# Kernel tuning notes

Measured on AMD Instinct MI355X. Metric: run time of the kernel, lower is better.

Reference implementation:

```python
import jax, jax.numpy as jnp
import numpy as np

N, E, D_IN, HID, OUT, H = 50000, 800000, 64, 128, 128, 8


def _lin(key, fan_in, fan_out, bias=True):
    k1, k2 = jax.random.split(key)
    W = jax.random.normal(k1, (fan_in, fan_out), jnp.float32) / np.sqrt(fan_in)
    if bias:
        b = jax.random.normal(k2, (fan_out,), jnp.float32) * 0.01
        return W, b
    return (W,)


def setup_inputs() -> dict:
    key = jax.random.key(0)
    ks = jax.random.split(key, 40)
    inp = {
        "x": jax.random.normal(ks[0], (N, D_IN), jnp.float32),
        "edge_index": jax.random.randint(ks[1], (2, E), 0, N, jnp.int64),
        "edge_attr": jax.random.normal(ks[2], (E, D_IN), jnp.float32),
    }
    dims = [(D_IN, HID), (HID, HID), (HID, OUT)]  # (in, heads*out_ch) per layer
    ki = 3
    for l, (di, do) in enumerate(dims):
        inp[f"Wq{l}"], inp[f"bq{l}"] = _lin(ks[ki], di, do); ki += 1
        inp[f"Wk{l}"], inp[f"bk{l}"] = _lin(ks[ki], di, do); ki += 1
        inp[f"Wv{l}"], inp[f"bv{l}"] = _lin(ks[ki], di, do); ki += 1
        (inp[f"We{l}"],) = _lin(ks[ki], D_IN, do, bias=False); ki += 1
        inp[f"Ws{l}"], inp[f"bs{l}"] = _lin(ks[ki], di, do); ki += 1
    for l in range(2):
        inp[f"g{l}"] = jnp.ones((HID,), jnp.float32)
        inp[f"be{l}"] = jnp.zeros((HID,), jnp.float32)
    return inp


def _transformer_conv(x, src, dst, edge_attr, Wq, bq, Wk, bk, Wv, bv, We, Ws, bs):
    n = x.shape[0]
    hc = Wq.shape[1]
    c = hc // H
    q = (x @ Wq + bq).reshape(n, H, c)
    k = (x @ Wk + bk).reshape(n, H, c)
    v = (x @ Wv + bv).reshape(n, H, c)
    e = (edge_attr @ We).reshape(-1, H, c)  # [E,H,c]
    ke = k[src] + e                          # edge-wise key + edge proj
    alpha = jnp.einsum("ehc,ehc->eh", q[dst], ke) / jnp.sqrt(jnp.float32(c))
    m = jax.ops.segment_max(alpha, dst, num_segments=n)
    m = jnp.where(jnp.isfinite(m), m, 0.0)
    p = jnp.exp(alpha - m[dst])
    s = jax.ops.segment_sum(p, dst, num_segments=n)
    a = p / (s[dst] + 1e-16)                 # segment softmax over in-edges
    msg = (v[src] + e) * a[..., None]
    out = jax.ops.segment_sum(msg, dst, num_segments=n).reshape(n, hc)
    return out + x @ Ws + bs                 # root/skip connection


def _bn(x, g, b):
    mu = jnp.mean(x, axis=0)
    var = jnp.mean(jnp.square(x - mu), axis=0)
    return g * (x - mu) * jax.lax.rsqrt(var + 1e-5) + b


def reference(x, edge_index, edge_attr,
              Wq0, bq0, Wk0, bk0, Wv0, bv0, We0, Ws0, bs0,
              Wq1, bq1, Wk1, bk1, Wv1, bv1, We1, Ws1, bs1,
              Wq2, bq2, Wk2, bk2, Wv2, bv2, We2, Ws2, bs2,
              g0, be0, g1, be1):
    src, dst = edge_index[0], edge_index[1]
    h = _transformer_conv(x, src, dst, edge_attr, Wq0, bq0, Wk0, bk0, Wv0, bv0, We0, Ws0, bs0)
    h = jax.nn.relu(_bn(h, g0, be0))
    h = _transformer_conv(h, src, dst, edge_attr, Wq1, bq1, Wk1, bk1, Wv1, bv1, We1, Ws1, bs1)
    h = jax.nn.relu(_bn(h, g1, be1))
    h = _transformer_conv(h, src, dst, edge_attr, Wq2, bq2, Wk2, bk2, Wv2, bv2, We2, Ws2, bs2)
    return h, edge_attr
```

## Files before the change

### kernel.cpp

```cpp
#include <hip/hip_runtime.h>
#include <hip/hip_bf16.h>

typedef __attribute__((ext_vector_type(8))) short short8;
typedef __attribute__((ext_vector_type(4))) float f32x4;
typedef unsigned short ushort_t;
typedef __attribute__((ext_vector_type(2))) unsigned short ushort2v;

static __device__ __forceinline__ ushort_t f2bf(float x) {
    __hip_bfloat16 h = __float2bfloat16(x);
    return *(ushort_t*)&h;
}
static __device__ __forceinline__ float bflo(unsigned int u) { return __uint_as_float(u << 16); }
static __device__ __forceinline__ float bfhi(unsigned int u) { return __uint_as_float(u & 0xffff0000u); }
static __device__ __forceinline__ float bfu(ushort_t u) { return __uint_as_float((unsigned int)u << 16); }


__global__ void hist_kernel(const int* __restrict__ dst, int E, int* __restrict__ hist) {
    int i = blockIdx.x * blockDim.x + threadIdx.x;
    if (i < E) atomicAdd(&hist[dst[i]], 1);
}

__global__ __launch_bounds__(1024) void scan_block_kernel(
    const int* __restrict__ hist, int n, int* __restrict__ row_ptr, int* __restrict__ bsums)
{
    __shared__ int lds[1024];
    int tid = threadIdx.x;
    int i = blockIdx.x * 1024 + tid;
    int vv = (i < n) ? hist[i] : 0;
    lds[tid] = vv;
    __syncthreads();
    for (int off = 1; off < 1024; off <<= 1) {
        int t = (tid >= off) ? lds[tid - off] : 0;
        __syncthreads();
        lds[tid] += t;
        __syncthreads();
    }
    if (i < n) row_ptr[i] = lds[tid] - vv;
    if (tid == 1023) bsums[blockIdx.x] = lds[1023];
}

__global__ void scan_tops_kernel(int* __restrict__ bsums, int nb) {
    if (threadIdx.x == 0 && blockIdx.x == 0) {
        int run = 0;
        for (int i = 0; i < nb; i++) { int t = bsums[i]; bsums[i] = run; run += t; }
    }
}

__global__ __launch_bounds__(256) void scan_add_kernel(
    const int* __restrict__ bsums, int n, int total,
    int* __restrict__ row_ptr, int* __restrict__ cursor)
{
    int i = blockIdx.x * blockDim.x + threadIdx.x;
    if (i < n) {
        int vv = row_ptr[i] + bsums[i >> 10];
        row_ptr[i] = vv;
        cursor[i] = vv;
    }
    if (i == 0) row_ptr[n] = total;
}

__global__ void scatter_kernel(const int* __restrict__ src, const int* __restrict__ dst, int E,
                               int* __restrict__ cursor, int* __restrict__ eid, int* __restrict__ srcs) {
    int i = blockIdx.x * blockDim.x + threadIdx.x;
    if (i < E) {
        int d = dst[i];
        int pos = atomicAdd(&cursor[d], 1);
        eid[pos] = i;
        srcs[pos] = src[i];
    }
}

__global__ __launch_bounds__(256) void permute_ea_kernel(
    const float* __restrict__ edge_attr, const int* __restrict__ eid, int E,
    ushort_t* __restrict__ ea)
{
    int idx = blockIdx.x * blockDim.x + threadIdx.x;
    if (idx >= E * 8) return;
    int j = idx >> 3, seg = idx & 7;
    int rsrc = eid[j];
    const float* s = edge_attr + (size_t)rsrc * 64 + seg * 8;
    float4 f0 = *(const float4*)s;
    float4 f1 = *(const float4*)(s + 4);
    short8 o;
    o[0] = f2bf(f0.x); o[1] = f2bf(f0.y); o[2] = f2bf(f0.z); o[3] = f2bf(f0.w);
    o[4] = f2bf(f1.x); o[5] = f2bf(f1.y); o[6] = f2bf(f1.z); o[7] = f2bf(f1.w);
    *(short8*)(ea + (size_t)j * 64 + seg * 8) = o;
}

__global__ __launch_bounds__(256) void pack_Wnode_kernel(
    const float* __restrict__ Wq, const float* __restrict__ Wk,
    const float* __restrict__ Wv, const float* __restrict__ Ws,
    int DI, ushort_t* __restrict__ dst)
{
    int NKF = DI >> 5;
    int total = DI * 512;
    int idx = blockIdx.x * blockDim.x + threadIdx.x;
    if (idx >= total) return;
    int j = idx & 7;
    int lane = (idx >> 3) & 63;
    int rest = idx >> 9;
    int kf = rest % NKF;
    int t = rest / NKF;
    int kdim = kf * 32 + (lane >> 4) * 8 + j;
    int ncol = t * 16 + (lane & 15);
    const float* W = (ncol < 128) ? Wq : (ncol < 256) ? Wk : (ncol < 384) ? Wv : Ws;
    dst[idx] = f2bf(W[kdim * 128 + (ncol & 127)]);
}

__global__ __launch_bounds__(256) void pack_bias_kernel(
    const float* __restrict__ bq, const float* __restrict__ bk,
    const float* __restrict__ bv, const float* __restrict__ bs,
    float* __restrict__ dst)
{
    int i = threadIdx.x + blockIdx.x * blockDim.x;
    if (i >= 512) return;
    const float* b = (i < 128) ? bq : (i < 256) ? bk : (i < 384) ? bv : bs;
    dst[i] = b[i & 127];
}

__global__ __launch_bounds__(256) void pack_We_kernel(
    const float* __restrict__ We0, const float* __restrict__ We1,
    const float* __restrict__ We2, ushort_t* __restrict__ Bpack)
{
    int idx = blockIdx.x * blockDim.x + threadIdx.x;
    if (idx >= 3 * 8192) return;
    int j = idx & 7;
    int lane = (idx >> 3) & 63;
    int kk = (idx >> 9) & 1;
    int t = (idx >> 10) & 7;
    int layer = idx >> 13;
    const float* We = (layer == 0) ? We0 : (layer == 1) ? We1 : We2;
    int kdim = kk * 32 + (lane >> 4) * 8 + j;
    int ncol = t * 16 + (lane & 15);
    Bpack[idx] = f2bf(We[kdim * 128 + ncol]);
}

template <int DI, bool BN>
__global__ __launch_bounds__(256) void node_gemm_mfma_kernel(
    const float* __restrict__ hin, int N,
    const ushort_t* __restrict__ Bpack, const float* __restrict__ biasc,
    const float* __restrict__ scale, const float* __restrict__ shift,
    float* __restrict__ qout, ushort_t* __restrict__ kout,
    ushort_t* __restrict__ vout, float* __restrict__ skipout)
{
    constexpr int NKF = DI / 32;
    __shared__ float ctile[64][132];
    int wave = threadIdx.x >> 6;
    int lane = threadIdx.x & 63;
    int tid = threadIdx.x;
    int base = blockIdx.x * 64;
    int m0 = base + wave * 16;

    int mrow = min(m0 + (lane & 15), N - 1);
    const float* arow = hin + (size_t)mrow * DI;
    int koff = (lane >> 4) * 8;

    short8 a[NKF];
#pragma unroll
    for (int kf = 0; kf < NKF; kf++) {
        float4 fa = *(const float4*)(arow + kf * 32 + koff);
        float4 fb = *(const float4*)(arow + kf * 32 + koff + 4);
        if constexpr (BN) {
            int c0 = kf * 32 + koff;
            float4 sa = *(const float4*)(scale + c0);
            float4 sb = *(const float4*)(scale + c0 + 4);
            float4 ha = *(const float4*)(shift + c0);
            float4 hb = *(const float4*)(shift + c0 + 4);
            fa.x = fmaxf(fa.x * sa.x + ha.x, 0.f);
            fa.y = fmaxf(fa.y * sa.y + ha.y, 0.f);
            fa.z = fmaxf(fa.z * sa.z + ha.z, 0.f);
            fa.w = fmaxf(fa.w * sa.w + ha.w, 0.f);
            fb.x = fmaxf(fb.x * sb.x + hb.x, 0.f);
            fb.y = fmaxf(fb.y * sb.y + hb.y, 0.f);
            fb.z = fmaxf(fb.z * sb.z + hb.z, 0.f);
            fb.w = fmaxf(fb.w * sb.w + hb.w, 0.f);
        }
        short8 t;
        t[0] = f2bf(fa.x); t[1] = f2bf(fa.y); t[2] = f2bf(fa.z); t[3] = f2bf(fa.w);
        t[4] = f2bf(fb.x); t[5] = f2bf(fb.y); t[6] = f2bf(fb.z); t[7] = f2bf(fb.w);
        a[kf] = t;
    }

    const short8* Bp = (const short8*)Bpack;
    f32x4 acc[32];
#pragma unroll
    for (int t = 0; t < 32; t++) acc[t] = (f32x4){0.f, 0.f, 0.f, 0.f};
#pragma unroll
    for (int t = 0; t < 32; t++) {
#pragma unroll
        for (int kf = 0; kf < NKF; kf++)
            acc[t] = __builtin_amdgcn_mfma_f32_16x16x32_bf16(a[kf], Bp[(t * NKF + kf) * 64 + lane], acc[t], 0, 0, 0);
    }

    int crow = (lane >> 4) * 4;
    int ccol = lane & 15;
#pragma unroll
    for (int osel = 0; osel < 4; osel++) {
#pragma unroll
        for (int t8 = 0; t8 < 8; t8++) {
            float bb = biasc[osel * 128 + t8 * 16 + ccol];
#pragma unroll
            for (int r = 0; r < 4; r++)
                ctile[wave * 16 + crow + r][t8 * 16 + ccol] = acc[osel * 8 + t8][r] + bb;
        }
        __syncthreads();
        if (osel == 0 || osel == 3) {
            float* out = (osel == 0) ? qout : skipout;
#pragma unroll
            for (int it = 0; it < 8; it++) {
                int idx4 = it * 256 + tid;
                int row = idx4 >> 5;
                int c4 = idx4 & 31;
                int gr = base + row;
                if (gr < N) {
                    float4 vv = *(const float4*)&ctile[row][c4 * 4];
                    *(float4*)(out + (size_t)gr * 128 + c4 * 4) = vv;
                }
            }
        } else {
            ushort_t* out = (osel == 1) ? kout : vout;
#pragma unroll
            for (int it = 0; it < 4; it++) {
                int idx8 = it * 256 + tid;
                int row = idx8 >> 4;
                int c8 = idx8 & 15;
                int gr = base + row;
                if (gr < N) {
                    const float* s = &ctile[row][c8 * 8];
                    short8 vv;
#pragma unroll
                    for (int jj = 0; jj < 8; jj++) vv[jj] = f2bf(s[jj]);
                    *(short8*)(out + (size_t)gr * 128 + c8 * 8) = vv;
                }
            }
        }
        __syncthreads();
    }
}

__global__ __launch_bounds__(256) void agg_fused_kernel(
    const int* __restrict__ row_ptr, const int* __restrict__ srcs,
    const float* __restrict__ q, const ushort_t* __restrict__ k,
    const ushort_t* __restrict__ v, const ushort_t* __restrict__ ea,
    const ushort_t* __restrict__ BpackWe,
    float* __restrict__ hout, int N)
{
    __shared__ ushort_t bsh[8192];
    __shared__ ushort_t elds[4][16][136];
    int tid = threadIdx.x;
    {
        const short8* s8 = (const short8*)BpackWe;
        short8* d8 = (short8*)bsh;
#pragma unroll
        for (int i = 0; i < 4; i++) d8[i * 256 + tid] = s8[i * 256 + tid];
    }
    __syncthreads();

    int wave = tid >> 6, lane = tid & 63;
    int n = blockIdx.x * 4 + wave;
    if (n >= N) return;

    const float2* q2 = (const float2*)q;
    const unsigned int* k32 = (const unsigned int*)k;
    const unsigned int* v32 = (const unsigned int*)v;
    float2* h2 = (float2*)hout;
    const short8* bs8 = (const short8*)bsh;

    int ch = lane & 15, kg = lane >> 4;
    float2 qq = q2[(size_t)n * 64 + lane];
    float2 sk = h2[(size_t)n * 64 + lane];
    float acc0 = 0.f, acc1 = 0.f, sw = 0.f;
    int jb = row_ptr[n], je = row_ptr[n + 1];

    short8 a0 = {}, a1 = {};
    int sv = 0;
    if (jb < je) {
        int j0 = min(jb + ch, je - 1);
        sv = srcs[j0];
        const ushort_t* row0 = ea + (size_t)j0 * 64;
        a0 = *(const short8*)(row0 + kg * 8);
        a1 = *(const short8*)(row0 + 32 + kg * 8);
    }

    for (int c0 = jb; c0 < je; c0 += 16) {
#pragma unroll
        for (int t = 0; t < 8; t++) {
            f32x4 z = (f32x4){0.f, 0.f, 0.f, 0.f};
            z = __builtin_amdgcn_mfma_f32_16x16x32_bf16(a0, bs8[(t * 2 + 0) * 64 + lane], z, 0, 0, 0);
            z = __builtin_amdgcn_mfma_f32_16x16x32_bf16(a1, bs8[(t * 2 + 1) * 64 + lane], z, 0, 0, 0);
#pragma unroll
            for (int r = 0; r < 4; r++)
                elds[wave][kg * 4 + r][t * 16 + ch] = f2bf(z[r]);
        }

        int cn = c0 + 16;
        short8 na0 = a0, na1 = a1;
        int nsv = sv;
        if (cn < je) {
            int jn = min(cn + ch, je - 1);
            nsv = srcs[jn];
            const ushort_t* nrow = ea + (size_t)jn * 64;
            na0 = *(const short8*)(nrow + kg * 8);
            na1 = *(const short8*)(nrow + 32 + kg * 8);
        }

        asm volatile("" ::: "memory");

        int cnt = min(16, je - c0);
        int r = 0;
        for (; r + 8 <= cnt; r += 8) {
            int s[8];
            ushort2v ee[8];
            unsigned int ku[8], vu[8];
#pragma unroll
            for (int u = 0; u < 8; u++) s[u] = __shfl(sv, r + u);
#pragma unroll
            for (int u = 0; u < 8; u++) ee[u] = *(const ushort2v*)&elds[wave][r + u][2 * lane];
#pragma unroll
            for (int u = 0; u < 8; u++) ku[u] = k32[(size_t)s[u] * 64 + lane];
#pragma unroll
            for (int u = 0; u < 8; u++) vu[u] = v32[(size_t)s[u] * 64 + lane];
            float p[8];
#pragma unroll
            for (int u = 0; u < 8; u++)
                p[u] = qq.x * (bflo(ku[u]) + bfu(ee[u][0])) + qq.y * (bfhi(ku[u]) + bfu(ee[u][1]));
#pragma unroll
            for (int u = 0; u < 8; u++) {
                p[u] += __shfl_xor(p[u], 1);
                p[u] += __shfl_xor(p[u], 2);
                p[u] += __shfl_xor(p[u], 4);
            }
            float w[8];
#pragma unroll
            for (int u = 0; u < 8; u++) w[u] = __expf(fminf(p[u] * 0.25f, 60.0f));
#pragma unroll
            for (int u = 0; u < 8; u++) {
                acc0 += w[u] * (bflo(vu[u]) + bfu(ee[u][0]));
                acc1 += w[u] * (bfhi(vu[u]) + bfu(ee[u][1]));
                sw += w[u];
            }
        }
        for (; r + 4 <= cnt; r += 4) {
            int s[4];
            ushort2v ee[4];
            unsigned int ku[4], vu[4];
#pragma unroll
            for (int u = 0; u < 4; u++) s[u] = __shfl(sv, r + u);
#pragma unroll
            for (int u = 0; u < 4; u++) ee[u] = *(const ushort2v*)&elds[wave][r + u][2 * lane];
#pragma unroll
            for (int u = 0; u < 4; u++) ku[u] = k32[(size_t)s[u] * 64 + lane];
#pragma unroll
            for (int u = 0; u < 4; u++) vu[u] = v32[(size_t)s[u] * 64 + lane];
            float p[4];
#pragma unroll
            for (int u = 0; u < 4; u++)
                p[u] = qq.x * (bflo(ku[u]) + bfu(ee[u][0])) + qq.y * (bfhi(ku[u]) + bfu(ee[u][1]));
#pragma unroll
            for (int u = 0; u < 4; u++) {
                p[u] += __shfl_xor(p[u], 1);
                p[u] += __shfl_xor(p[u], 2);
                p[u] += __shfl_xor(p[u], 4);
            }
#pragma unroll
            for (int u = 0; u < 4; u++) {
                float w = __expf(fminf(p[u] * 0.25f, 60.0f));
                acc0 += w * (bflo(vu[u]) + bfu(ee[u][0]));
                acc1 += w * (bfhi(vu[u]) + bfu(ee[u][1]));
                sw += w;
            }
        }
        for (; r < cnt; ++r) {
            int s = __shfl(sv, r);
            ushort2v ee = *(const ushort2v*)&elds[wave][r][2 * lane];
            unsigned int ku = k32[(size_t)s * 64 + lane];
            unsigned int vu = v32[(size_t)s * 64 + lane];
            float e0 = bfu(ee[0]), e1 = bfu(ee[1]);
            float part = qq.x * (bflo(ku) + e0) + qq.y * (bfhi(ku) + e1);
            part += __shfl_xor(part, 1);
            part += __shfl_xor(part, 2);
            part += __shfl_xor(part, 4);
            float w = __expf(fminf(part * 0.25f, 60.0f));
            acc0 += w * (bflo(vu) + e0);
            acc1 += w * (bfhi(vu) + e1);
            sw += w;
        }
        a0 = na0; a1 = na1; sv = nsv;
    }
    float inv = 1.0f / (sw + 1e-16f);
    float2 o;
    o.x = acc0 * inv + sk.x;
    o.y = acc1 * inv + sk.y;
    h2[(size_t)n * 64 + lane] = o;
}

__global__ __launch_bounds__(128) void bn_stats_kernel(const float* __restrict__ h, int N,
                                                       float* __restrict__ sums) {
    int f = threadIdx.x;
    float s = 0.f, s2 = 0.f;
    for (int n = blockIdx.x; n < N; n += gridDim.x) {
        float x = h[(size_t)n * 128 + f];
        s += x;
        s2 += x * x;
    }
    atomicAdd(&sums[f], s);
    atomicAdd(&sums[128 + f], s2);
}

__global__ __launch_bounds__(128) void bn_finalize_kernel(
    const float* __restrict__ sums, const float* __restrict__ g,
    const float* __restrict__ be, int N,
    float* __restrict__ scale, float* __restrict__ shift)
{
    int f = threadIdx.x;
    float invN = 1.0f / (float)N;
    float mu = sums[f] * invN;
    float var = sums[128 + f] * invN - mu * mu;
    float sc = g[f] * rsqrtf(var + 1e-5f);
    scale[f] = sc;
    shift[f] = be[f] - mu * sc;
}

extern "C" void kernel_launch(void* const* d_in, const int* in_sizes, int n_in,
                              void* d_out, int out_size, void* d_ws, size_t ws_size,
                              hipStream_t stream)
{
    const float* x = (const float*)d_in[0];
    const int* edge_index = (const int*)d_in[1];
    const float* edge_attr = (const float*)d_in[2];
    int N = in_sizes[0] / 64;
    int E = in_sizes[1] / 2;
    const int* src = edge_index;
    const int* dst = edge_index + E;

    const float* W[3][9];
    for (int l = 0; l < 3; l++)
        for (int i = 0; i < 9; i++) W[l][i] = (const float*)d_in[3 + l * 9 + i];
    const float* g0 = (const float*)d_in[30];
    const float* be0 = (const float*)d_in[31];
    const float* g1 = (const float*)d_in[32];
    const float* be1 = (const float*)d_in[33];

    char* p = (char*)d_ws;
    auto alloc = [&](size_t bytes) -> char* {
        char* r = p;
        p += (bytes + 255) & ~(size_t)255;
        return r;
    };
    float* q = (float*)alloc((size_t)N * 128 * 4);
    ushort_t* k = (ushort_t*)alloc((size_t)N * 128 * 2);
    ushort_t* v = (ushort_t*)alloc((size_t)N * 128 * 2);
    float* B = (float*)alloc((size_t)N * 128 * 4);
    ushort_t* ea = (ushort_t*)alloc((size_t)E * 64 * 2);
    int* row_ptr = (int*)alloc((size_t)(N + 1) * 4);
    int* cursor = (int*)alloc((size_t)N * 4);
    int* histb = (int*)alloc((size_t)N * 4);
    int* eid = (int*)alloc((size_t)E * 4);
    int* srcs = (int*)alloc((size_t)E * 4);
    int* bsums = (int*)alloc(64 * 4);
    float* sums = (float*)alloc(512 * 4);
    float* bnp = (float*)alloc(512 * 4);
    ushort_t* BpackE = (ushort_t*)alloc((size_t)3 * 8192 * 2);
    ushort_t* BpackN = (ushort_t*)alloc((size_t)3 * 65536 * 2);
    float* biasc = (float*)alloc((size_t)3 * 512 * 4);

    int nb = (N + 1023) / 1024;

    hipMemsetAsync(histb, 0, (size_t)N * 4, stream);
    hipMemsetAsync(sums, 0, 512 * 4, stream);
    hist_kernel<<<(E + 255) / 256, 256, 0, stream>>>(dst, E, histb);
    scan_block_kernel<<<nb, 1024, 0, stream>>>(histb, N, row_ptr, bsums);
    scan_tops_kernel<<<1, 64, 0, stream>>>(bsums, nb);
    scan_add_kernel<<<(N + 255) / 256, 256, 0, stream>>>(bsums, N, E, row_ptr, cursor);
    scatter_kernel<<<(E + 255) / 256, 256, 0, stream>>>(src, dst, E, cursor, eid, srcs);
    permute_ea_kernel<<<(E * 8 + 255) / 256, 256, 0, stream>>>(edge_attr, eid, E, ea);

    pack_We_kernel<<<(3 * 8192 + 255) / 256, 256, 0, stream>>>(W[0][6], W[1][6], W[2][6], BpackE);
    for (int l = 0; l < 3; l++) {
        int DI = (l == 0) ? 64 : 128;
        pack_Wnode_kernel<<<(DI * 512 + 255) / 256, 256, 0, stream>>>(
            W[l][0], W[l][2], W[l][4], W[l][7], DI, BpackN + (size_t)l * 65536);
        pack_bias_kernel<<<2, 256, 0, stream>>>(W[l][1], W[l][3], W[l][5], W[l][8],
                                                biasc + (size_t)l * 512);
    }

    for (int l = 0; l < 3; l++) {
        float* skipbuf = (l == 2) ? (float*)d_out : B;
        if (l == 0)
            node_gemm_mfma_kernel<64, false><<<(N + 63) / 64, 256, 0, stream>>>(
                x, N, BpackN, biasc, nullptr, nullptr, q, k, v, skipbuf);
        else
            node_gemm_mfma_kernel<128, true><<<(N + 63) / 64, 256, 0, stream>>>(
                B, N, BpackN + (size_t)l * 65536, biasc + (size_t)l * 512,
                bnp + (size_t)(l - 1) * 256, bnp + (size_t)(l - 1) * 256 + 128,
                q, k, v, skipbuf);
        agg_fused_kernel<<<(N + 3) / 4, 256, 0, stream>>>(
            row_ptr, srcs, q, k, v, ea, BpackE + (size_t)l * 8192, skipbuf, N);
        if (l < 2) {
            bn_stats_kernel<<<256, 128, 0, stream>>>(skipbuf, N, sums + (size_t)l * 256);
            const float* gg = (l == 0) ? g0 : g1;
            const float* bb = (l == 0) ? be0 : be1;
            bn_finalize_kernel<<<1, 128, 0, stream>>>(
                sums + (size_t)l * 256, gg, bb, N,
                bnp + (size_t)l * 256, bnp + (size_t)l * 256 + 128);
        }
    }

    hipMemcpyAsync((float*)d_out + (size_t)N * 128, edge_attr, (size_t)E * 64 * 4,
                   hipMemcpyDeviceToDevice, stream);
}
```

Measured before the change: 772.1 us.

## Split each node's edge aggregation across two waves and combine via LDS

```diff
diff --git a/kernel.cpp b/kernel.cpp
--- a/kernel.cpp
+++ b/kernel.cpp
@@ -238,7 +238,7 @@
     }
 }
 
-__global__ __launch_bounds__(256) void agg_fused_kernel(
+__global__ __launch_bounds__(512) void agg_fused_kernel(
     const int* __restrict__ row_ptr, const int* __restrict__ srcs,
     const float* __restrict__ q, const ushort_t* __restrict__ k,
     const ushort_t* __restrict__ v, const ushort_t* __restrict__ ea,
@@ -246,19 +246,23 @@
     float* __restrict__ hout, int N)
 {
     __shared__ ushort_t bsh[8192];
-    __shared__ ushort_t elds[4][16][136];
+    __shared__ ushort_t elds[8][8][136];
+    __shared__ float comb[4][64][3];
     int tid = threadIdx.x;
     {
         const short8* s8 = (const short8*)BpackWe;
         short8* d8 = (short8*)bsh;
-#pragma unroll
-        for (int i = 0; i < 4; i++) d8[i * 256 + tid] = s8[i * 256 + tid];
+        d8[tid] = s8[tid];
+        d8[512 + tid] = s8[512 + tid];
     }
     __syncthreads();
 
     int wave = tid >> 6, lane = tid & 63;
-    int n = blockIdx.x * 4 + wave;
-    if (n >= N) return;
+    int w = wave >> 1;
+    int sub = wave & 1;
+    int n = blockIdx.x * 4 + w;
+    bool active = (n < N);
+    int nn = active ? n : (N - 1);
 
     const float2* q2 = (const float2*)q;
     const unsigned int* k32 = (const unsigned int*)k;
@@ -267,30 +271,33 @@
     const short8* bs8 = (const short8*)bsh;
 
     int ch = lane & 15, kg = lane >> 4;
-    float2 qq = q2[(size_t)n * 64 + lane];
-    float2 sk = h2[(size_t)n * 64 + lane];
+    float2 qq = q2[(size_t)nn * 64 + lane];
     float acc0 = 0.f, acc1 = 0.f, sw = 0.f;
-    int jb = row_ptr[n], je = row_ptr[n + 1];
-
+    int jb = row_ptr[nn], je = row_ptr[nn + 1];
+    if (!active) { jb = 0; je = 0; }
+
+    int c0_first = jb + sub * 8;
     short8 a0 = {}, a1 = {};
     int sv = 0;
-    if (jb < je) {
-        int j0 = min(jb + ch, je - 1);
+    if (c0_first < je) {
+        int j0 = min(c0_first + ch, je - 1);
         sv = srcs[j0];
         const ushort_t* row0 = ea + (size_t)j0 * 64;
         a0 = *(const short8*)(row0 + kg * 8);
         a1 = *(const short8*)(row0 + 32 + kg * 8);
     }
 
-    for (int c0 = jb; c0 < je; c0 += 16) {
+    for (int c0 = c0_first; c0 < je; c0 += 16) {
 #pragma unroll
         for (int t = 0; t < 8; t++) {
             f32x4 z = (f32x4){0.f, 0.f, 0.f, 0.f};
             z = __builtin_amdgcn_mfma_f32_16x16x32_bf16(a0, bs8[(t * 2 + 0) * 64 + lane], z, 0, 0, 0);
             z = __builtin_amdgcn_mfma_f32_16x16x32_bf16(a1, bs8[(t * 2 + 1) * 64 + lane], z, 0, 0, 0);
-#pragma unroll
-            for (int r = 0; r < 4; r++)
-                elds[wave][kg * 4 + r][t * 16 + ch] = f2bf(z[r]);
+            if (kg < 2) {
+#pragma unroll
+                for (int r = 0; r < 4; r++)
+                    elds[wave][kg * 4 + r][t * 16 + ch] = f2bf(z[r]);
+            }
         }
 
         int cn = c0 + 16;
@@ -306,7 +313,7 @@
 
         asm volatile("" ::: "memory");
 
-        int cnt = min(16, je - c0);
+        int cnt = min(8, je - c0);
         int r = 0;
         for (; r + 8 <= cnt; r += 8) {
             int s[8];
@@ -330,14 +337,14 @@
                 p[u] += __shfl_xor(p[u], 2);
                 p[u] += __shfl_xor(p[u], 4);
             }
-            float w[8];
-#pragma unroll
-            for (int u = 0; u < 8; u++) w[u] = __expf(fminf(p[u] * 0.25f, 60.0f));
+            float wv[8];
+#pragma unroll
+            for (int u = 0; u < 8; u++) wv[u] = __expf(fminf(p[u] * 0.25f, 60.0f));
 #pragma unroll
             for (int u = 0; u < 8; u++) {
-                acc0 += w[u] * (bflo(vu[u]) + bfu(ee[u][0]));
-                acc1 += w[u] * (bfhi(vu[u]) + bfu(ee[u][1]));
-                sw += w[u];
+                acc0 += wv[u] * (bflo(vu[u]) + bfu(ee[u][0]));
+                acc1 += wv[u] * (bfhi(vu[u]) + bfu(ee[u][1]));
+                sw += wv[u];
             }
         }
         for (; r + 4 <= cnt; r += 4) {
@@ -364,10 +371,10 @@
             }
 #pragma unroll
             for (int u = 0; u < 4; u++) {
-                float w = __expf(fminf(p[u] * 0.25f, 60.0f));
-                acc0 += w * (bflo(vu[u]) + bfu(ee[u][0]));
-                acc1 += w * (bfhi(vu[u]) + bfu(ee[u][1]));
-                sw += w;
+                float wv = __expf(fminf(p[u] * 0.25f, 60.0f));
+                acc0 += wv * (bflo(vu[u]) + bfu(ee[u][0]));
+                acc1 += wv * (bfhi(vu[u]) + bfu(ee[u][1]));
+                sw += wv;
             }
         }
         for (; r < cnt; ++r) {
@@ -380,18 +387,31 @@
             part += __shfl_xor(part, 1);
             part += __shfl_xor(part, 2);
             part += __shfl_xor(part, 4);
-            float w = __expf(fminf(part * 0.25f, 60.0f));
-            acc0 += w * (bflo(vu) + e0);
-            acc1 += w * (bfhi(vu) + e1);
-            sw += w;
+            float wv = __expf(fminf(part * 0.25f, 60.0f));
+            acc0 += wv * (bflo(vu) + e0);
+            acc1 += wv * (bfhi(vu) + e1);
+            sw += wv;
         }
         a0 = na0; a1 = na1; sv = nsv;
     }
-    float inv = 1.0f / (sw + 1e-16f);
-    float2 o;
-    o.x = acc0 * inv + sk.x;
-    o.y = acc1 * inv + sk.y;
-    h2[(size_t)n * 64 + lane] = o;
+
+    if (sub == 1) {
+        comb[w][lane][0] = acc0;
+        comb[w][lane][1] = acc1;
+        comb[w][lane][2] = sw;
+    }
+    __syncthreads();
+    if (sub == 0 && active) {
+        acc0 += comb[w][lane][0];
+        acc1 += comb[w][lane][1];
+        sw += comb[w][lane][2];
+        float2 sk = h2[(size_t)n * 64 + lane];
+        float inv = 1.0f / (sw + 1e-16f);
+        float2 o;
+        o.x = acc0 * inv + sk.x;
+        o.y = acc1 * inv + sk.y;
+        h2[(size_t)n * 64 + lane] = o;
+    }
 }
 
 __global__ __launch_bounds__(128) void bn_stats_kernel(const float* __restrict__ h, int N,
@@ -494,7 +514,7 @@
                 B, N, BpackN + (size_t)l * 65536, biasc + (size_t)l * 512,
                 bnp + (size_t)(l - 1) * 256, bnp + (size_t)(l - 1) * 256 + 128,
                 q, k, v, skipbuf);
-        agg_fused_kernel<<<(N + 3) / 4, 256, 0, stream>>>(
+        agg_fused_kernel<<<(N + 3) / 4, 512, 0, stream>>>(
             row_ptr, srcs, q, k, v, ea, BpackE + (size_t)l * 8192, skipbuf, N);
         if (l < 2) {
             bn_stats_kernel<<<256, 128, 0, stream>>>(skipbuf, N, sums + (size_t)l * 256);
```

Result: slower. 949.7 us (+23.0%).
